# Performance work log

Hardware: AMD Instinct MI355X
Metric: run time of the kernel (lower is better)

## Reference

```python
import jax, jax.numpy as jnp
import numpy as np

N = 100000
E = 1600000
IN_C, HID_C, OUT_C = 40, 64, 3


def _sage_params(key, f_in, f_out):
    k1, k2, k3 = jax.random.split(key, 3)
    s = 1.0 / np.sqrt(f_in)
    return (jax.random.uniform(k1, (f_in, f_out), jnp.float32, -s, s),  # W_neigh (lin_l)
            jax.random.uniform(k2, (f_in, f_out), jnp.float32, -s, s),  # W_root  (lin_r)
            jax.random.uniform(k3, (f_out,), jnp.float32, -s, s))       # bias


def setup_inputs() -> dict:
    key = jax.random.key(0)
    ks = jax.random.split(key, 8)
    x = jax.random.normal(ks[0], (N, IN_C), jnp.float32)
    edge_index = jax.random.randint(ks[1], (2, E), 0, N, jnp.int64)
    dims = [(IN_C, HID_C), (HID_C, HID_C), (HID_C, OUT_C),   # encoder
            (OUT_C, HID_C), (HID_C, HID_C), (HID_C, IN_C)]   # decoder
    names = ['enc1', 'enc2', 'enc3', 'dec1', 'dec2', 'dec3']
    out = {'x': x, 'edge_index': edge_index}
    for name, (fi, fo), k in zip(names, dims, ks[2:]):
        Wl, Wr, b = _sage_params(k, fi, fo)
        out[name + '_Wl'] = Wl
        out[name + '_Wr'] = Wr
        out[name + '_b'] = b
    return out


def _sage_conv(h, src, dst, inv_deg, Wl, Wr, b):
    # mean-aggregate neighbor features (messages src -> dst), then linear.
    msg_sum = jax.ops.segment_sum(h[src], dst, num_segments=N)  # [N, F_in]
    agg = msg_sum * inv_deg                                      # mean aggregation
    return agg @ Wl + h @ Wr + b


def reference(x, edge_index,
              enc1_Wl, enc1_Wr, enc1_b, enc2_Wl, enc2_Wr, enc2_b,
              enc3_Wl, enc3_Wr, enc3_b, dec1_Wl, dec1_Wr, dec1_b,
              dec2_Wl, dec2_Wr, dec2_b, dec3_Wl, dec3_Wr, dec3_b):
    src, dst = edge_index[0], edge_index[1]
    deg = jax.ops.segment_sum(jnp.ones((E,), jnp.float32), dst, num_segments=N)
    inv_deg = (1.0 / jnp.maximum(deg, 1.0))[:, None]
    # encoder
    h = jax.nn.relu(_sage_conv(x, src, dst, inv_deg, enc1_Wl, enc1_Wr, enc1_b))
    h = jax.nn.relu(_sage_conv(h, src, dst, inv_deg, enc2_Wl, enc2_Wr, enc2_b))
    z = _sage_conv(h, src, dst, inv_deg, enc3_Wl, enc3_Wr, enc3_b)
    # decoder
    h = jax.nn.relu(_sage_conv(z, src, dst, inv_deg, dec1_Wl, dec1_Wr, dec1_b))
    h = jax.nn.relu(_sage_conv(h, src, dst, inv_deg, dec2_Wl, dec2_Wr, dec2_b))
    x_rec = _sage_conv(h, src, dst, inv_deg, dec3_Wl, dec3_Wr, dec3_b)
    return (x_rec, z)
```

## Files before the change

### kernel.cpp

```cpp
#include <hip/hip_runtime.h>
#include <stdint.h>

#define NNODES 100000
#define NEDGES 1600000
#define NB 98
#define WIN 25000
#define NSL 64
#define SLICE 25000

typedef unsigned short ushort_t;
typedef __attribute__((ext_vector_type(8))) short bf16x8;
typedef __attribute__((ext_vector_type(4))) float f32x4;

__device__ __forceinline__ float b2f(ushort_t u) {
  union { float f; uint32_t i; } v; v.i = ((uint32_t)u) << 16; return v.f;
}
__device__ __forceinline__ float blo(uint32_t p) {
  union { float f; uint32_t i; } v; v.i = p << 16; return v.f;
}
__device__ __forceinline__ float bhi(uint32_t p) {
  union { float f; uint32_t i; } v; v.i = p & 0xffff0000u; return v.f;
}
__device__ __forceinline__ ushort_t f2b(float f) {
  union { float f; uint32_t i; } v; v.f = f;
  uint32_t r = (v.i + 0x7fffu + ((v.i >> 16) & 1u)) >> 16;
  return (ushort_t)r;
}
__device__ __forceinline__ uint32_t pack2(float lo, float hi) {
  return (uint32_t)f2b(lo) | ((uint32_t)f2b(hi) << 16);
}
__device__ __forceinline__ int clampn(int i) {
  return i < 0 ? 0 : (i >= NNODES ? NNODES - 1 : i);
}

__global__ void detect_k(const uint32_t* __restrict__ x, const uint32_t* __restrict__ ei,
                         int* __restrict__ flags) {
  if (blockIdx.x == 0 && threadIdx.x == 0) {
    int cf = 0, ci = 0;
    for (int i = 0; i < 256; ++i) {
      uint32_t u = x[i];
      uint32_t e = (u >> 7) & 0xFFu;
      if (e >= 100u && e <= 141u) cf++;
      if (ei[2 * i + 1] == 0u) ci++;
    }
    flags[0] = (cf >= 128) ? 1 : 0;
    flags[1] = (ci >= 128) ? 1 : 0;
  }
}

__global__ void zero_i32(int* __restrict__ p, int n) {
  int i = blockIdx.x * blockDim.x + threadIdx.x;
  if (i < n) p[i] = 0;
}

__global__ void cvt_e32_k(const uint32_t* __restrict__ ei, int* __restrict__ src32,
                          int* __restrict__ dst32, const int* __restrict__ flags) {
  int e = blockIdx.x * blockDim.x + threadIdx.x;
  if (e >= NEDGES) return;
  int s, d;
  if (flags[1]) {
    s = (int)ei[2 * (size_t)e];
    d = (int)ei[2 * (size_t)NEDGES + 2 * (size_t)e];
  } else {
    s = (int)ei[e];
    d = (int)ei[(size_t)NEDGES + e];
  }
  src32[e] = clampn(s);
  dst32[e] = clampn(d);
}

__global__ __launch_bounds__(1024) void histw2_k(const int* __restrict__ dst32,
                                                 int* __restrict__ degp) {
  __shared__ int h[WIN];
  int b = blockIdx.x;
  int w = b >> 6, s = b & 63;
  for (int j = threadIdx.x; j < WIN; j += 1024) h[j] = 0;
  __syncthreads();
  int base = w * WIN;
  int e0 = s * SLICE, e1 = e0 + SLICE;
  for (int e = e0 + threadIdx.x; e < e1; e += 1024) {
    int j = dst32[e] - base;
    if ((unsigned)j < (unsigned)WIN) atomicAdd(&h[j], 1);
  }
  __syncthreads();
  int* dp = degp + (size_t)s * NNODES + base;
  for (int j = threadIdx.x; j < WIN; j += 1024) dp[j] = h[j];
}

__global__ void hreduce_k(int* __restrict__ degp, int* __restrict__ deg) {
  int n = blockIdx.x * blockDim.x + threadIdx.x;
  if (n >= NNODES) return;
  int run = 0;
  for (int s = 0; s < NSL; ++s) {
    size_t idx = (size_t)s * NNODES + n;
    int t = degp[idx];
    degp[idx] = run;
    run += t;
  }
  deg[n] = run;
}

__global__ __launch_bounds__(1024) void scan1_k(const int* __restrict__ deg, int* __restrict__ bsum) {
  __shared__ int wsum[16];
  int tid = threadIdx.x;
  int i = blockIdx.x * 1024 + tid;
  int v = (i < NNODES) ? deg[i] : 0;
  #pragma unroll
  for (int d = 32; d >= 1; d >>= 1) v += __shfl_down(v, d);
  if ((tid & 63) == 0) wsum[tid >> 6] = v;
  __syncthreads();
  if (tid == 0) {
    int t = 0;
    #pragma unroll
    for (int w = 0; w < 16; ++w) t += wsum[w];
    bsum[blockIdx.x] = t;
  }
}

__global__ void scan2_k(int* __restrict__ bsum, int* __restrict__ offs) {
  if (blockIdx.x == 0 && threadIdx.x == 0) {
    int run = 0;
    for (int b = 0; b < NB; ++b) { int t = bsum[b]; bsum[b] = run; run += t; }
    offs[NNODES] = run;
  }
}

__global__ __launch_bounds__(1024) void scan3_k(const int* __restrict__ deg, const int* __restrict__ bsum,
                                                int* __restrict__ offs, int* __restrict__ cursor,
                                                float* __restrict__ invd) {
  __shared__ int wsum[16];
  int tid = threadIdx.x;
  int lane = tid & 63, wid = tid >> 6;
  int i = blockIdx.x * 1024 + tid;
  int v = (i < NNODES) ? deg[i] : 0;
  int s = v;
  #pragma unroll
  for (int d = 1; d < 64; d <<= 1) {
    int t = __shfl_up(s, d);
    if (lane >= d) s += t;
  }
  if (lane == 63) wsum[wid] = s;
  __syncthreads();
  int wprefix = 0;
  #pragma unroll
  for (int w = 0; w < 16; ++w)
    if (w < wid) wprefix += wsum[w];
  if (i < NNODES) {
    int excl = bsum[blockIdx.x] + wprefix + s - v;
    offs[i] = excl;
    cursor[i] = excl;
    invd[i] = 1.0f / fmaxf((float)v, 1.0f);
  }
}

__global__ void scatter4_k(const int* __restrict__ src32, const int* __restrict__ dst32,
                           int* __restrict__ cursor, int* __restrict__ csr,
                           int lo, int hi) {
  int e = blockIdx.x * blockDim.x + threadIdx.x;
  if (e >= NEDGES) return;
  int d = dst32[e];
  if (d < lo || d >= hi) return;
  int p = atomicAdd(&cursor[d], 1);
  if (p >= 0 && p < NEDGES) csr[p] = src32[e];
}

template <bool BF16>
__global__ void cvt_packx_k(const void* __restrict__ src, uint32_t* __restrict__ dst, int npairs,
                            const int* __restrict__ flags) {
  if (flags[0] != (BF16 ? 1 : 0)) return;
  int i = blockIdx.x * blockDim.x + threadIdx.x;
  if (i < npairs) {
    if constexpr (BF16) dst[i] = ((const uint32_t*)src)[i];
    else {
      const float* s = (const float*)src;
      dst[i] = pack2(s[2 * i], s[2 * i + 1]);
    }
  }
}

template <bool BF16>
__global__ void cvt_outp_k(const uint32_t* __restrict__ src, void* __restrict__ dst, int npairs,
                           const int* __restrict__ flags) {
  if (flags[0] != (BF16 ? 1 : 0)) return;
  int i = blockIdx.x * blockDim.x + threadIdx.x;
  if (i < npairs) {
    if constexpr (BF16) ((uint32_t*)dst)[i] = src[i];
    else {
      uint32_t w = src[i];
      float* d = (float*)dst;
      d[2 * i] = blo(w);
      d[2 * i + 1] = bhi(w);
    }
  }
}

template <bool BF16>
__global__ void cvt_out_k(const float* __restrict__ src, void* __restrict__ dst, int n,
                          const int* __restrict__ flags) {
  if (flags[0] != (BF16 ? 1 : 0)) return;
  int i = blockIdx.x * blockDim.x + threadIdx.x;
  if (i < n) {
    if constexpr (BF16) ((ushort_t*)dst)[i] = f2b(src[i]);
    else ((float*)dst)[i] = src[i];
  }
}

struct WPtrs { const void* p[18]; int sz[18]; int off[18]; };

template <bool BF16>
__global__ void cvt_w_k(WPtrs w, float* __restrict__ dst, const int* __restrict__ flags) {
  if (flags[0] != (BF16 ? 1 : 0)) return;
  int a = blockIdx.x;
  int sz = w.sz[a], off = w.off[a];
  for (int t = threadIdx.x; t < sz; t += blockDim.x) {
    dst[off + t] = BF16 ? b2f(((const ushort_t*)w.p[a])[t]) : ((const float*)w.p[a])[t];
  }
}

template <bool ADD_U>
__global__ __launch_bounds__(256) void agg3_k(const float* __restrict__ feat, const int* __restrict__ csr,
                                              const int* __restrict__ offs, const float* __restrict__ invd,
                                              const float* __restrict__ u, float* __restrict__ out) {
  int n = blockIdx.x * blockDim.x + threadIdx.x;
  if (n >= NNODES) return;
  int k0 = offs[n], k1 = offs[n + 1];
  float a0 = 0.f, a1 = 0.f, a2 = 0.f;
  int k = k0;
  for (; k + 4 <= k1; k += 4) {
    const float* r0 = feat + (size_t)clampn(csr[k]) * 3;
    const float* r1 = feat + (size_t)clampn(csr[k + 1]) * 3;
    const float* r2 = feat + (size_t)clampn(csr[k + 2]) * 3;
    const float* r3 = feat + (size_t)clampn(csr[k + 3]) * 3;
    a0 += r0[0] + r1[0] + r2[0] + r3[0];
    a1 += r0[1] + r1[1] + r2[1] + r3[1];
    a2 += r0[2] + r1[2] + r2[2] + r3[2];
  }
  for (; k < k1; ++k) {
    const float* r = feat + (size_t)clampn(csr[k]) * 3;
    a0 += r[0]; a1 += r[1]; a2 += r[2];
  }
  float iv = invd[n];
  a0 *= iv; a1 *= iv; a2 *= iv;
  if constexpr (ADD_U) {
    a0 += u[(size_t)n * 3];
    a1 += u[(size_t)n * 3 + 1];
    a2 += u[(size_t)n * 3 + 2];
  }
  out[(size_t)n * 3]     = a0;
  out[(size_t)n * 3 + 1] = a1;
  out[(size_t)n * 3 + 2] = a2;
}

template <int PAIRS, bool ADD_U>
__global__ __launch_bounds__(256) void aggp4_k(const uint32_t* __restrict__ feat, const int* __restrict__ csr,
                                               const int* __restrict__ offs, const float* __restrict__ invd,
                                               const uint32_t* __restrict__ u, uint32_t* __restrict__ out) {
  constexpr int HP = PAIRS / 2;
  int lane = threadIdx.x & 63;
  int n = (blockIdx.x * blockDim.x + threadIdx.x) >> 6;
  if (n >= NNODES) return;
  int q = lane >> 4;
  int p = lane & 15;
  int k0 = offs[n], k1 = offs[n + 1];
  float a0 = 0.f, a1 = 0.f, a2 = 0.f, a3 = 0.f;
  int k = k0;
  for (; k + 8 <= k1; k += 8) {
    int r0 = clampn(csr[k + q]);
    int r1 = clampn(csr[k + 4 + q]);
    if (p < HP) {
      uint2 w0 = ((const uint2*)(feat + (size_t)r0 * PAIRS))[p];
      uint2 w1 = ((const uint2*)(feat + (size_t)r1 * PAIRS))[p];
      a0 += blo(w0.x) + blo(w1.x);
      a1 += bhi(w0.x) + bhi(w1.x);
      a2 += blo(w0.y) + blo(w1.y);
      a3 += bhi(w0.y) + bhi(w1.y);
    }
  }
  for (; k + 4 <= k1; k += 4) {
    int r0 = clampn(csr[k + q]);
    if (p < HP) {
      uint2 w0 = ((const uint2*)(feat + (size_t)r0 * PAIRS))[p];
      a0 += blo(w0.x); a1 += bhi(w0.x); a2 += blo(w0.y); a3 += bhi(w0.y);
    }
  }
  int rem = k1 - k;
  if (q < rem && p < HP) {
    int r0 = clampn(csr[k + q]);
    uint2 w0 = ((const uint2*)(feat + (size_t)r0 * PAIRS))[p];
    a0 += blo(w0.x); a1 += bhi(w0.x); a2 += blo(w0.y); a3 += bhi(w0.y);
  }
  a0 += __shfl_xor(a0, 16); a0 += __shfl_xor(a0, 32);
  a1 += __shfl_xor(a1, 16); a1 += __shfl_xor(a1, 32);
  a2 += __shfl_xor(a2, 16); a2 += __shfl_xor(a2, 32);
  a3 += __shfl_xor(a3, 16); a3 += __shfl_xor(a3, 32);
  if (q == 0 && p < HP) {
    float iv = invd[n];
    float v0 = a0 * iv, v1 = a1 * iv, v2 = a2 * iv, v3 = a3 * iv;
    if constexpr (ADD_U) {
      uint2 uw = ((const uint2*)(u + (size_t)n * PAIRS))[p];
      v0 += blo(uw.x); v1 += bhi(uw.x); v2 += blo(uw.y); v3 += bhi(uw.y);
    }
    uint2 ow;
    ow.x = pack2(v0, v1);
    ow.y = pack2(v2, v3);
    ((uint2*)(out + (size_t)n * PAIRS))[p] = ow;
  }
}

template <int F_IN, int F_OUT, bool DUAL, bool RELU, bool PIN, bool POUT>
__global__ __launch_bounds__(256) void mgemm_k(const void* __restrict__ Av, const void* __restrict__ Bv,
                                               const float* __restrict__ W1, const float* __restrict__ W2,
                                               const float* __restrict__ Wb,
                                               void* __restrict__ C1v, void* __restrict__ C2v) {
  constexpr int KS = (F_IN + 31) / 32;
  constexpr int JT = (F_OUT + 15) / 16;
  constexpr int PP = F_IN / 2;
  int lane = threadIdx.x & 63;
  int wid  = threadIdx.x >> 6;
  int tile = blockIdx.x * 4 + wid;
  if (tile * 16 >= NNODES) return;
  int l15 = lane & 15, l4 = lane >> 4;

  bf16x8 w1f[KS][JT], w2f[KS][JT];
  float bv[JT];
  #pragma unroll
  for (int ks = 0; ks < KS; ++ks) {
    #pragma unroll
    for (int jt = 0; jt < JT; ++jt) {
      int col = jt * 16 + l15;
      #pragma unroll
      for (int j = 0; j < 8; ++j) {
        int k = ks * 32 + l4 * 8 + j;
        bool ok = (k < F_IN) && (col < F_OUT);
        w1f[ks][jt][j] = ok ? (short)f2b(W1[k * F_OUT + col]) : (short)0;
        w2f[ks][jt][j] = ok ? (short)f2b(W2[k * F_OUT + col]) : (short)0;
      }
    }
  }
  #pragma unroll
  for (int jt = 0; jt < JT; ++jt) {
    int col = jt * 16 + l15;
    bv[jt] = (col < F_OUT) ? Wb[col] : 0.f;
  }

  int row = tile * 16 + l15;
  bf16x8 af[KS], bfr[KS];
  if constexpr (PIN) {
    const uint32_t* Arow = (const uint32_t*)Av + (size_t)row * PP;
    #pragma unroll
    for (int ks = 0; ks < KS; ++ks) {
      #pragma unroll
      for (int w4 = 0; w4 < 4; ++w4) {
        int word = ks * 16 + l4 * 4 + w4;
        uint32_t v = (word < PP) ? Arow[word] : 0u;
        af[ks][2 * w4]     = (short)(v & 0xffffu);
        af[ks][2 * w4 + 1] = (short)(v >> 16);
      }
    }
    if constexpr (!DUAL) {
      const uint32_t* Brow = (const uint32_t*)Bv + (size_t)row * PP;
      #pragma unroll
      for (int ks = 0; ks < KS; ++ks) {
        #pragma unroll
        for (int w4 = 0; w4 < 4; ++w4) {
          int word = ks * 16 + l4 * 4 + w4;
          uint32_t v = (word < PP) ? Brow[word] : 0u;
          bfr[ks][2 * w4]     = (short)(v & 0xffffu);
          bfr[ks][2 * w4 + 1] = (short)(v >> 16);
        }
      }
    }
  } else {
    const float* Arow = (const float*)Av + (size_t)row * F_IN;
    #pragma unroll
    for (int ks = 0; ks < KS; ++ks) {
      #pragma unroll
      for (int j = 0; j < 8; ++j) {
        int k = ks * 32 + l4 * 8 + j;
        af[ks][j] = (k < F_IN) ? (short)f2b(Arow[k]) : (short)0;
      }
    }
    if constexpr (!DUAL) {
      const float* Brow = (const float*)Bv + (size_t)row * F_IN;
      #pragma unroll
      for (int ks = 0; ks < KS; ++ks) {
        #pragma unroll
        for (int j = 0; j < 8; ++j) {
          int k = ks * 32 + l4 * 8 + j;
          bfr[ks][j] = (k < F_IN) ? (short)f2b(Brow[k]) : (short)0;
        }
      }
    }
  }

  f32x4 acc1[JT], acc2[DUAL ? JT : 1];
  #pragma unroll
  for (int jt = 0; jt < JT; ++jt) {
    acc1[jt] = (f32x4)(0.f);
    if constexpr (DUAL) acc2[jt] = (f32x4)(0.f);
  }

  #pragma unroll
  for (int ks = 0; ks < KS; ++ks) {
    #pragma unroll
    for (int jt = 0; jt < JT; ++jt) {
      acc1[jt] = __builtin_amdgcn_mfma_f32_16x16x32_bf16(af[ks], w1f[ks][jt], acc1[jt], 0, 0, 0);
      if constexpr (DUAL)
        acc2[jt] = __builtin_amdgcn_mfma_f32_16x16x32_bf16(af[ks], w2f[ks][jt], acc2[jt], 0, 0, 0);
      else
        acc1[jt] = __builtin_amdgcn_mfma_f32_16x16x32_bf16(bfr[ks], w2f[ks][jt], acc1[jt], 0, 0, 0);
    }
  }

  #pragma unroll
  for (int jt = 0; jt < JT; ++jt) {
    int col = jt * 16 + l15;
    #pragma unroll
    for (int r = 0; r < 4; ++r) {
      int orow = tile * 16 + l4 * 4 + r;
      if constexpr (DUAL) {
        float v1 = acc1[jt][r];
        float v2 = acc2[jt][r] + bv[jt];
        if constexpr (POUT) {
          float p1 = __shfl_xor(v1, 1);
          float p2 = __shfl_xor(v2, 1);
          if (((lane & 1) == 0) && col < F_OUT) {
            ((uint32_t*)C1v)[(size_t)orow * (F_OUT / 2) + (col >> 1)] = pack2(v1, p1);
            ((uint32_t*)C2v)[(size_t)orow * (F_OUT / 2) + (col >> 1)] = pack2(v2, p2);
          }
        } else {
          if (col < F_OUT) {
            ((float*)C1v)[(size_t)orow * F_OUT + col] = v1;
            ((float*)C2v)[(size_t)orow * F_OUT + col] = v2;
          }
        }
      } else {
        float v = acc1[jt][r] + bv[jt];
        if constexpr (RELU) v = fmaxf(v, 0.f);
        if constexpr (POUT) {
          float pv = __shfl_xor(v, 1);
          if (((lane & 1) == 0) && col < F_OUT)
            ((uint32_t*)C1v)[(size_t)orow * (F_OUT / 2) + (col >> 1)] = pack2(v, pv);
        } else {
          if (col < F_OUT)
            ((float*)C1v)[(size_t)orow * F_OUT + col] = v;
        }
      }
    }
  }
}

extern "C" void kernel_launch(void* const* d_in, const int* in_sizes, int n_in,
                              void* d_out, int out_size, void* d_ws, size_t ws_size,
                              hipStream_t stream) {
  const uint32_t* xw = (const uint32_t*)d_in[0];
  const uint32_t* ei = (const uint32_t*)d_in[1];

  char* ws = (char*)d_ws;
  size_t off = 0;
  auto carve = [&](size_t bytes) -> char* {
    char* p = ws + off;
    off = (off + bytes + 255) & ~(size_t)255;
    return p;
  };
  int* flags     = (int*)carve(8);
  int* deg       = (int*)carve((size_t)NNODES * 4);
  int* offs      = (int*)carve((size_t)(NNODES + 1) * 4);
  int* cursor    = (int*)carve((size_t)NNODES * 4);
  float* invd    = (float*)carve((size_t)NNODES * 4);
  int* bsum      = (int*)carve((size_t)NB * 4);
  int* csr       = (int*)carve((size_t)NEDGES * 4);
  float* wf      = (float*)carve((size_t)32768 * 4);
  uint32_t* xp   = (uint32_t*)carve((size_t)NNODES * 20 * 4);
  uint32_t* mp   = (uint32_t*)carve((size_t)NNODES * 20 * 4);
  uint32_t* b0p  = (uint32_t*)carve((size_t)NNODES * 32 * 4);
  uint32_t* b1p  = (uint32_t*)carve((size_t)NNODES * 32 * 4);
  uint32_t* b2p  = (uint32_t*)carve((size_t)NNODES * 32 * 4);
  uint32_t* y40p = (uint32_t*)carve((size_t)NNODES * 20 * 4);
  uint32_t* u40p = (uint32_t*)carve((size_t)NNODES * 20 * 4);
  uint32_t* xrp  = (uint32_t*)carve((size_t)NNODES * 20 * 4);
  float* y3f     = (float*)carve((size_t)NNODES * 3 * 4);
  float* u3f     = (float*)carve((size_t)NNODES * 3 * 4);
  float* zf      = (float*)carve((size_t)NNODES * 3 * 4);
  float* m3f     = (float*)carve((size_t)NNODES * 3 * 4);

  int* degp = (int*)b0p;
  int* src32 = (int*)b2p;
  int* dst32 = src32 + NEDGES;

  static const int wsz[18] = {2560, 2560, 64, 4096, 4096, 64, 192, 192, 3,
                              192, 192, 64, 4096, 4096, 64, 2560, 2560, 40};
  WPtrs wp;
  int woff = 0;
  for (int i = 0; i < 18; ++i) {
    wp.p[i] = d_in[2 + i];
    wp.sz[i] = wsz[i];
    wp.off[i] = woff;
    woff += wsz[i];
  }
  const float* W[18];
  for (int i = 0; i < 18; ++i) W[i] = wf + wp.off[i];

  detect_k<<<1, 64, 0, stream>>>(xw, ei, flags);
  const int EB = (NEDGES + 255) / 256;
  cvt_e32_k<<<EB, 256, 0, stream>>>(ei, src32, dst32, flags);
  zero_i32<<<EB, 256, 0, stream>>>(csr, NEDGES);
  histw2_k<<<4 * NSL, 1024, 0, stream>>>(dst32, degp);
  hreduce_k<<<(NNODES + 255) / 256, 256, 0, stream>>>(degp, deg);
  scan1_k<<<NB, 1024, 0, stream>>>(deg, bsum);
  scan2_k<<<1, 64, 0, stream>>>(bsum, offs);
  scan3_k<<<NB, 1024, 0, stream>>>(deg, bsum, offs, cursor, invd);
  scatter4_k<<<EB, 256, 0, stream>>>(src32, dst32, cursor, csr, 0, 25000);
  scatter4_k<<<EB, 256, 0, stream>>>(src32, dst32, cursor, csr, 25000, 50000);
  scatter4_k<<<EB, 256, 0, stream>>>(src32, dst32, cursor, csr, 50000, 75000);
  scatter4_k<<<EB, 256, 0, stream>>>(src32, dst32, cursor, csr, 75000, 100000);

  const int NXP = NNODES * 20;
  cvt_packx_k<false><<<(NXP + 255) / 256, 256, 0, stream>>>(d_in[0], xp, NXP, flags);
  cvt_packx_k<true ><<<(NXP + 255) / 256, 256, 0, stream>>>(d_in[0], xp, NXP, flags);
  cvt_w_k<false><<<18, 256, 0, stream>>>(wp, wf, flags);
  cvt_w_k<true ><<<18, 256, 0, stream>>>(wp, wf, flags);

  const int AGGW_BLOCKS = (NNODES * 64 + 255) / 256;
  const int AGG3_BLOCKS = (NNODES + 255) / 256;
  const int MG = (NNODES / 16 + 3) / 4;

  aggp4_k<20, false><<<AGGW_BLOCKS, 256, 0, stream>>>(xp, csr, offs, invd, nullptr, mp);
  mgemm_k<40, 64, false, true, true, true><<<MG, 256, 0, stream>>>(mp, xp, W[0], W[1], W[2], b1p, nullptr);
  aggp4_k<32, false><<<AGGW_BLOCKS, 256, 0, stream>>>(b1p, csr, offs, invd, nullptr, b0p);
  mgemm_k<64, 64, false, true, true, true><<<MG, 256, 0, stream>>>(b0p, b1p, W[3], W[4], W[5], b2p, nullptr);
  mgemm_k<64, 3, true, false, true, false><<<MG, 256, 0, stream>>>(b2p, nullptr, W[6], W[7], W[8], y3f, u3f);
  agg3_k<true><<<AGG3_BLOCKS, 256, 0, stream>>>(y3f, csr, offs, invd, u3f, zf);
  agg3_k<false><<<AGG3_BLOCKS, 256, 0, stream>>>(zf, csr, offs, invd, nullptr, m3f);
  mgemm_k<3, 64, false, true, false, true><<<MG, 256, 0, stream>>>(m3f, zf, W[9], W[10], W[11], b1p, nullptr);
  aggp4_k<32, false><<<AGGW_BLOCKS, 256, 0, stream>>>(b1p, csr, offs, invd, nullptr, b0p);
  mgemm_k<64, 64, false, true, true, true><<<MG, 256, 0, stream>>>(b0p, b1p, W[12], W[13], W[14], b2p, nullptr);
  mgemm_k<64, 40, true, false, true, true><<<MG, 256, 0, stream>>>(b2p, nullptr, W[15], W[16], W[17], y40p, u40p);
  aggp4_k<20, true><<<AGGW_BLOCKS, 256, 0, stream>>>(y40p, csr, offs, invd, u40p, xrp);

  const int NX = NNODES * 40;
  const int NZ = NNODES * 3;
  cvt_outp_k<false><<<(NXP + 255) / 256, 256, 0, stream>>>(xrp, d_out, NXP, flags);
  cvt_outp_k<true ><<<(NXP + 255) / 256, 256, 0, stream>>>(xrp, d_out, NXP, flags);
  cvt_out_k<false><<<(NZ + 255) / 256, 256, 0, stream>>>(zf, (float*)d_out + NX, NZ, flags);
  cvt_out_k<true ><<<(NZ + 255) / 256, 256, 0, stream>>>(zf, (ushort_t*)d_out + NX, NZ, flags);
  (void)in_sizes; (void)n_in; (void)out_size; (void)ws_size;
}
```

Before: 501.4 us.

## Slice 64-wide hidden features into 8 column slabs for cache-local aggregation

Hidden 64-channel bf16 activations are now stored as 8 slabs of 8 channels each (16 bytes per node per slab), written directly by the GEMM epilogue and read by a new slab aggregation kernel. Each block processes one slab, with 16 neighbors times 4 words per wavefront, so the random gathers touch a 1.6 MB table that fits in cache instead of the full 12.8 MB row-major array. The GEMMs read the slab layout with 16-byte loads. In exchange the GEMM stores become strided across slabs, and the aggregation loop is grid-strided over a fixed 2048 blocks, which could load-balance poorly.

```diff
diff --git a/kernel.cpp b/kernel.cpp
--- a/kernel.cpp
+++ b/kernel.cpp
@@ -307,7 +307,42 @@
   }
 }
 
-template <int F_IN, int F_OUT, bool DUAL, bool RELU, bool PIN, bool POUT>
+__global__ __launch_bounds__(256) void aggs_k(const uint32_t* __restrict__ tblS, const int* __restrict__ csr,
+                                              const int* __restrict__ offs, const float* __restrict__ invd,
+                                              uint32_t* __restrict__ outS) {
+  int b = blockIdx.x;
+  int s = b & 7;
+  int wid = threadIdx.x >> 6;
+  int lane = threadIdx.x & 63;
+  int v = (b >> 3) * 4 + wid;
+  int nb = lane >> 2;
+  int w = lane & 3;
+  const uint32_t* tbl = tblS + (size_t)s * NNODES * 4;
+  uint32_t* out = outS + (size_t)s * NNODES * 4;
+  for (int n = v; n < NNODES; n += 1024) {
+    int k0 = offs[n], k1 = offs[n + 1];
+    float aL = 0.f, aH = 0.f;
+    int k = k0;
+    for (; k + 16 <= k1; k += 16) {
+      int r = clampn(csr[k + nb]);
+      uint32_t x = tbl[(size_t)r * 4 + w];
+      aL += blo(x); aH += bhi(x);
+    }
+    if (k + nb < k1) {
+      int r = clampn(csr[k + nb]);
+      uint32_t x = tbl[(size_t)r * 4 + w];
+      aL += blo(x); aH += bhi(x);
+    }
+    aL += __shfl_xor(aL, 4); aL += __shfl_xor(aL, 8); aL += __shfl_xor(aL, 16); aL += __shfl_xor(aL, 32);
+    aH += __shfl_xor(aH, 4); aH += __shfl_xor(aH, 8); aH += __shfl_xor(aH, 16); aH += __shfl_xor(aH, 32);
+    if (lane < 4) {
+      float iv = invd[n];
+      out[(size_t)n * 4 + w] = pack2(aL * iv, aH * iv);
+    }
+  }
+}
+
+template <int F_IN, int F_OUT, bool DUAL, bool RELU, int AL, int BL, int OUTL>
 __global__ __launch_bounds__(256) void mgemm_k(const void* __restrict__ Av, const void* __restrict__ Bv,
                                                const float* __restrict__ W1, const float* __restrict__ W2,
                                                const float* __restrict__ Wb,
@@ -345,53 +380,44 @@
 
   int row = tile * 16 + l15;
   bf16x8 af[KS], bfr[KS];
-  if constexpr (PIN) {
-    const uint32_t* Arow = (const uint32_t*)Av + (size_t)row * PP;
-    #pragma unroll
-    for (int ks = 0; ks < KS; ++ks) {
+
+  auto loadfrag = [&](const void* Pv, bf16x8 (&fr)[KS], auto layout) {
+    constexpr int L = decltype(layout)::value;
+    if constexpr (L == 2) {
       #pragma unroll
-      for (int w4 = 0; w4 < 4; ++w4) {
-        int word = ks * 16 + l4 * 4 + w4;
-        uint32_t v = (word < PP) ? Arow[word] : 0u;
-        af[ks][2 * w4]     = (short)(v & 0xffffu);
-        af[ks][2 * w4 + 1] = (short)(v >> 16);
+      for (int ks = 0; ks < KS; ++ks) {
+        uint4 vv = *(const uint4*)((const uint32_t*)Pv + ((size_t)(ks * 4 + l4) * NNODES + row) * 4);
+        fr[ks][0] = (short)(vv.x & 0xffffu); fr[ks][1] = (short)(vv.x >> 16);
+        fr[ks][2] = (short)(vv.y & 0xffffu); fr[ks][3] = (short)(vv.y >> 16);
+        fr[ks][4] = (short)(vv.z & 0xffffu); fr[ks][5] = (short)(vv.z >> 16);
+        fr[ks][6] = (short)(vv.w & 0xffffu); fr[ks][7] = (short)(vv.w >> 16);
       }
-    }
-    if constexpr (!DUAL) {
-      const uint32_t* Brow = (const uint32_t*)Bv + (size_t)row * PP;
+    } else if constexpr (L == 1) {
+      const uint32_t* Prow = (const uint32_t*)Pv + (size_t)row * PP;
       #pragma unroll
       for (int ks = 0; ks < KS; ++ks) {
         #pragma unroll
         for (int w4 = 0; w4 < 4; ++w4) {
           int word = ks * 16 + l4 * 4 + w4;
-          uint32_t v = (word < PP) ? Brow[word] : 0u;
-          bfr[ks][2 * w4]     = (short)(v & 0xffffu);
-          bfr[ks][2 * w4 + 1] = (short)(v >> 16);
+          uint32_t v = (word < PP) ? Prow[word] : 0u;
+          fr[ks][2 * w4]     = (short)(v & 0xffffu);
+          fr[ks][2 * w4 + 1] = (short)(v >> 16);
         }
       }
-    }
-  } else {
-    const float* Arow = (const float*)Av + (size_t)row * F_IN;
-    #pragma unroll
-    for (int ks = 0; ks < KS; ++ks) {
-      #pragma unroll
-      for (int j = 0; j < 8; ++j) {
-        int k = ks * 32 + l4 * 8 + j;
-        af[ks][j] = (k < F_IN) ? (short)f2b(Arow[k]) : (short)0;
-      }
-    }
-    if constexpr (!DUAL) {
-      const float* Brow = (const float*)Bv + (size_t)row * F_IN;
+    } else {
+      const float* Prow = (const float*)Pv + (size_t)row * F_IN;
       #pragma unroll
       for (int ks = 0; ks < KS; ++ks) {
         #pragma unroll
         for (int j = 0; j < 8; ++j) {
           int k = ks * 32 + l4 * 8 + j;
-          bfr[ks][j] = (k < F_IN) ? (short)f2b(Brow[k]) : (short)0;
+          fr[ks][j] = (k < F_IN) ? (short)f2b(Prow[k]) : (short)0;
         }
       }
     }
-  }
+  };
+  loadfrag(Av, af, std::integral_constant<int, AL>{});
+  if constexpr (!DUAL) loadfrag(Bv, bfr, std::integral_constant<int, BL>{});
 
   f32x4 acc1[JT], acc2[DUAL ? JT : 1];
   #pragma unroll
@@ -412,6 +438,20 @@
     }
   }
 
+  auto store1 = [&](void* Cv, float vv, int orow, int col, float pv) {
+    if constexpr (OUTL == 2) {
+      int wo = col >> 1;
+      if (((lane & 1) == 0) && col < F_OUT)
+        ((uint32_t*)Cv)[((size_t)(wo >> 2) * NNODES + orow) * 4 + (wo & 3)] = pack2(vv, pv);
+    } else if constexpr (OUTL == 1) {
+      if (((lane & 1) == 0) && col < F_OUT)
+        ((uint32_t*)Cv)[(size_t)orow * (F_OUT / 2) + (col >> 1)] = pack2(vv, pv);
+    } else {
+      if (col < F_OUT)
+        ((float*)Cv)[(size_t)orow * F_OUT + col] = vv;
+    }
+  };
+
   #pragma unroll
   for (int jt = 0; jt < JT; ++jt) {
     int col = jt * 16 + l15;
@@ -421,30 +461,15 @@
       if constexpr (DUAL) {
         float v1 = acc1[jt][r];
         float v2 = acc2[jt][r] + bv[jt];
-        if constexpr (POUT) {
-          float p1 = __shfl_xor(v1, 1);
-          float p2 = __shfl_xor(v2, 1);
-          if (((lane & 1) == 0) && col < F_OUT) {
-            ((uint32_t*)C1v)[(size_t)orow * (F_OUT / 2) + (col >> 1)] = pack2(v1, p1);
-            ((uint32_t*)C2v)[(size_t)orow * (F_OUT / 2) + (col >> 1)] = pack2(v2, p2);
-          }
-        } else {
-          if (col < F_OUT) {
-            ((float*)C1v)[(size_t)orow * F_OUT + col] = v1;
-            ((float*)C2v)[(size_t)orow * F_OUT + col] = v2;
-          }
-        }
+        float p1 = (OUTL != 0) ? __shfl_xor(v1, 1) : 0.f;
+        float p2 = (OUTL != 0) ? __shfl_xor(v2, 1) : 0.f;
+        store1(C1v, v1, orow, col, p1);
+        store1(C2v, v2, orow, col, p2);
       } else {
         float v = acc1[jt][r] + bv[jt];
         if constexpr (RELU) v = fmaxf(v, 0.f);
-        if constexpr (POUT) {
-          float pv = __shfl_xor(v, 1);
-          if (((lane & 1) == 0) && col < F_OUT)
-            ((uint32_t*)C1v)[(size_t)orow * (F_OUT / 2) + (col >> 1)] = pack2(v, pv);
-        } else {
-          if (col < F_OUT)
-            ((float*)C1v)[(size_t)orow * F_OUT + col] = v;
-        }
+        float pv = (OUTL != 0) ? __shfl_xor(v, 1) : 0.f;
+        store1(C1v, v, orow, col, pv);
       }
     }
   }
@@ -522,20 +547,21 @@
   cvt_w_k<true ><<<18, 256, 0, stream>>>(wp, wf, flags);
 
   const int AGGW_BLOCKS = (NNODES * 64 + 255) / 256;
+  const int AGGS_BLOCKS = 2048;
   const int AGG3_BLOCKS = (NNODES + 255) / 256;
   const int MG = (NNODES / 16 + 3) / 4;
 
   aggp4_k<20, false><<<AGGW_BLOCKS, 256, 0, stream>>>(xp, csr, offs, invd, nullptr, mp);
-  mgemm_k<40, 64, false, true, true, true><<<MG, 256, 0, stream>>>(mp, xp, W[0], W[1], W[2], b1p, nullptr);
-  aggp4_k<32, false><<<AGGW_BLOCKS, 256, 0, stream>>>(b1p, csr, offs, invd, nullptr, b0p);
-  mgemm_k<64, 64, false, true, true, true><<<MG, 256, 0, stream>>>(b0p, b1p, W[3], W[4], W[5], b2p, nullptr);
-  mgemm_k<64, 3, true, false, true, false><<<MG, 256, 0, stream>>>(b2p, nullptr, W[6], W[7], W[8], y3f, u3f);
+  mgemm_k<40, 64, false, true, 1, 1, 2><<<MG, 256, 0, stream>>>(mp, xp, W[0], W[1], W[2], b1p, nullptr);
+  aggs_k<<<AGGS_BLOCKS, 256, 0, stream>>>(b1p, csr, offs, invd, b0p);
+  mgemm_k<64, 64, false, true, 2, 2, 2><<<MG, 256, 0, stream>>>(b0p, b1p, W[3], W[4], W[5], b2p, nullptr);
+  mgemm_k<64, 3, true, false, 2, 0, 0><<<MG, 256, 0, stream>>>(b2p, nullptr, W[6], W[7], W[8], y3f, u3f);
   agg3_k<true><<<AGG3_BLOCKS, 256, 0, stream>>>(y3f, csr, offs, invd, u3f, zf);
   agg3_k<false><<<AGG3_BLOCKS, 256, 0, stream>>>(zf, csr, offs, invd, nullptr, m3f);
-  mgemm_k<3, 64, false, true, false, true><<<MG, 256, 0, stream>>>(m3f, zf, W[9], W[10], W[11], b1p, nullptr);
-  aggp4_k<32, false><<<AGGW_BLOCKS, 256, 0, stream>>>(b1p, csr, offs, invd, nullptr, b0p);
-  mgemm_k<64, 64, false, true, true, true><<<MG, 256, 0, stream>>>(b0p, b1p, W[12], W[13], W[14], b2p, nullptr);
-  mgemm_k<64, 40, true, false, true, true><<<MG, 256, 0, stream>>>(b2p, nullptr, W[15], W[16], W[17], y40p, u40p);
+  mgemm_k<3, 64, false, true, 0, 0, 2><<<MG, 256, 0, stream>>>(m3f, zf, W[9], W[10], W[11], b1p, nullptr);
+  aggs_k<<<AGGS_BLOCKS, 256, 0, stream>>>(b1p, csr, offs, invd, b0p);
+  mgemm_k<64, 64, false, true, 2, 2, 2><<<MG, 256, 0, stream>>>(b0p, b1p, W[12], W[13], W[14], b2p, nullptr);
+  mgemm_k<64, 40, true, false, 2, 0, 1><<<MG, 256, 0, stream>>>(b2p, nullptr, W[15], W[16], W[17], y40p, u40p);
   aggp4_k<20, true><<<AGGW_BLOCKS, 256, 0, stream>>>(y40p, csr, offs, invd, u40p, xrp);
 
   const int NX = NNODES * 40;
```

Result: slower. 704.3 us (+40.5%).
